# Kernel tuning notes

Measured on AMD Instinct MI355X. Metric: run time of the kernel, lower is better.

Reference implementation:

```python
import jax, jax.numpy as jnp
import numpy as np

N_EMBD = 1024
BLOCK_SIZE = 2048
ATTN_SPAN = 256
LN_EPS = 1e-5


def _band_mask(T, span, dtype):
    ones = jnp.ones((T, T), dtype=dtype)
    # tril(.,0) * (1 - tril(.,-span)) -> causal band of width `span`
    return jnp.tril(ones, 0) * (1.0 - jnp.tril(ones, -span))


def setup_inputs() -> dict:
    key = jax.random.key(0)
    k_x, k_w, k_b, k_lw = jax.random.split(key, 4)
    B, T, C = 4, BLOCK_SIZE, N_EMBD
    x = jax.random.normal(k_x, (B, T, C), dtype=jnp.float32)
    # qkv_net: Linear(C, 3C) with bias (torch default)
    lim = 1.0 / np.sqrt(C)
    W_qkv = jax.random.uniform(k_w, (C, 3 * C), minval=-lim, maxval=lim, dtype=jnp.float32)
    b_qkv = jax.random.uniform(k_b, (3 * C,), minval=-lim, maxval=lim, dtype=jnp.float32)
    ln_w = jnp.ones((C,), dtype=jnp.float32)
    ln_b = jnp.zeros((C,), dtype=jnp.float32)
    return {"x": x, "W_qkv": W_qkv, "b_qkv": b_qkv, "ln_w": ln_w, "ln_b": ln_b}


def _layer_norm(h, w, b):
    mu = jnp.mean(h, axis=-1, keepdims=True)
    var = jnp.var(h, axis=-1, keepdims=True)
    return (h - mu) * jax.lax.rsqrt(var + LN_EPS) * w + b


def reference(x, W_qkv, b_qkv, ln_w, ln_b):
    B, T, C = x.shape
    qkv = x @ W_qkv + b_qkv  # [B,T,3C]
    q, k, v = jnp.split(qkv, 3, axis=-1)
    scale = np.sqrt(C * ATTN_SPAN).astype(np.float32)
    scores = jnp.einsum('bid,bjd->bij', q, k) / scale  # [B,T,T]
    scores = scores * _band_mask(T, ATTN_SPAN, x.dtype)[None, :, :]
    out = jnp.einsum('bij,bjd->bid', scores, v)  # [B,T,C]
    return _layer_norm(out, ln_w, ln_b)
```

## Files before the change

kernel.cpp:

```cpp
#include <hip/hip_runtime.h>
#include <cstdint>
#include <cstddef>

#define N_EMBD 1024
#define T_SEQ  2048
#define NBATCH 4
#define SPAN   256
#define C3     3072

typedef float  floatx4 __attribute__((ext_vector_type(4)));
typedef __bf16 bf16x8  __attribute__((ext_vector_type(8)));

__device__ inline unsigned short f2bf(float f) {
    union { float f; unsigned u; } x; x.f = f;
    unsigned u = x.u;
    unsigned r = (u + 0x7fffu + ((u >> 16) & 1u)) >> 16;
    return (unsigned short)r;
}

typedef __attribute__((address_space(1))) const void GVOID;
typedef __attribute__((address_space(3))) void LVOID;
__device__ inline void gl2lds16(const void* g, void* l) {
    __builtin_amdgcn_global_load_lds((GVOID*)g, (LVOID*)l, 16, 0, 0);
}

__device__ inline void stage128x32(const unsigned short* g, size_t stride,
                                   unsigned short* lds, int lane, int wave) {
    const int r     = wave * 16 + (lane >> 2);
    const int chunk = (lane & 3) ^ ((r >> 1) & 3);
    const unsigned short* src = g + (size_t)r * stride + chunk * 8;
    gl2lds16(src,               &lds[(wave * 16) * 32]);
    gl2lds16(src + 64 * stride, &lds[(64 + wave * 16) * 32]);
}

__device__ inline void stage64x64(const unsigned short* g, size_t stride,
                                  unsigned short* lds, int lane, int wave) {
#pragma unroll
    for (int rnd = 0; rnd < 2; rnd++) {
        const int r = rnd * 32 + wave * 8 + (lane >> 3);
        const int chunk = (lane & 7) ^ (r & 7);
        gl2lds16(g + (size_t)r * stride + chunk * 8, &lds[(rnd * 32 + wave * 8) * 64]);
    }
}

__device__ inline void stage128x64(const unsigned short* g, size_t stride,
                                   unsigned short* lds, int lane, int wave) {
#pragma unroll
    for (int rnd = 0; rnd < 4; rnd++) {
        const int r = rnd * 32 + wave * 8 + (lane >> 3);
        const int chunk = (lane & 7) ^ (r & 7);
        gl2lds16(g + (size_t)r * stride + chunk * 8, &lds[(rnd * 32 + wave * 8) * 64]);
    }
}

__global__ __launch_bounds__(256) void k_prep(const float* __restrict__ x,
                                              unsigned short* __restrict__ Xb,
                                              const float* __restrict__ W,
                                              unsigned short* __restrict__ WbT) {
    __shared__ unsigned short t[32][33];
    if (blockIdx.x < 8192) {
        int i = (blockIdx.x * 256 + threadIdx.x) * 4;
        float4 v = *(const float4*)(x + i);
        ushort4 o;
        o.x = f2bf(v.x); o.y = f2bf(v.y); o.z = f2bf(v.z); o.w = f2bf(v.w);
        *(ushort4*)(Xb + i) = o;
    } else {
        int bid = blockIdx.x - 8192;
        int k0 = (bid & 31) * 32, n0 = (bid >> 5) * 32;
        int tx = threadIdx.x & 31, ty = threadIdx.x >> 5;
#pragma unroll
        for (int i = 0; i < 4; i++) {
            int k = k0 + ty + i * 8;
            t[ty + i * 8][tx] = f2bf(W[(size_t)k * C3 + n0 + tx]);
        }
        __syncthreads();
#pragma unroll
        for (int i = 0; i < 4; i++) {
            int n = n0 + ty + i * 8;
            WbT[(size_t)n * N_EMBD + k0 + tx] = t[tx][ty + i * 8];
        }
    }
}

__global__ __launch_bounds__(256) void k_gemm(const unsigned short* __restrict__ Xb,
                                              const unsigned short* __restrict__ WbT,
                                              const float* __restrict__ bqkv,
                                              unsigned short* __restrict__ QK,
                                              unsigned short* __restrict__ Vt) {
    __shared__ unsigned short As[4096];
    __shared__ unsigned short Bs[4096];
    const int tid = threadIdx.x, lane = tid & 63, wave = tid >> 6;
    const int bx = blockIdx.x, m0 = blockIdx.y * 128;
    const bool isV = (bx >= 16);
    const int n0 = isV ? (2048 + (bx - 16) * 128) : (bx * 128);
    const int wr = wave >> 1, wc = wave & 1;

    floatx4 acc[4][4] = {};

    const unsigned short* gA = (isV ? WbT + (size_t)n0 * N_EMBD : Xb  + (size_t)m0 * N_EMBD);
    const unsigned short* gB = (isV ? Xb  + (size_t)m0 * N_EMBD : WbT + (size_t)n0 * N_EMBD);
    const int qk = ((lane >> 4) ^ ((lane >> 1) & 3)) * 8;
    const int ra = wr * 64 + (lane & 15);
    const int rb = wc * 64 + (lane & 15);

    for (int k0 = 0; k0 < N_EMBD; k0 += 32) {
        stage128x32(gA + k0, N_EMBD, As, lane, wave);
        stage128x32(gB + k0, N_EMBD, Bs, lane, wave);
        __syncthreads();
        bf16x8 a[4], b[4];
#pragma unroll
        for (int mi = 0; mi < 4; mi++) a[mi] = *(const bf16x8*)&As[(ra + mi * 16) * 32 + qk];
#pragma unroll
        for (int ni = 0; ni < 4; ni++) b[ni] = *(const bf16x8*)&Bs[(rb + ni * 16) * 32 + qk];
#pragma unroll
        for (int mi = 0; mi < 4; mi++)
#pragma unroll
            for (int ni = 0; ni < 4; ni++)
                acc[mi][ni] = __builtin_amdgcn_mfma_f32_16x16x32_bf16(a[mi], b[ni], acc[mi][ni], 0, 0, 0);
        __syncthreads();
    }

    const int cn = lane & 15, q = lane >> 4;
    unsigned short* base = isV ? Vt : QK;
    const int rowbase = isV ? (((m0 >> 11) << 10) + (n0 - 2048)) : m0;
    const int colbase = isV ? (m0 & 2047) : n0;
#pragma unroll
    for (int mi = 0; mi < 4; mi++) {
#pragma unroll
        for (int r = 0; r < 4; r++) {
            const int arow = wr * 64 + mi * 16 + q * 4 + r;
            unsigned short* dst = base + (size_t)(rowbase + arow) * 2048 + colbase;
#pragma unroll
            for (int ni = 0; ni < 4; ni++) {
                const int acol = wc * 64 + ni * 16 + cn;
                const float bias = bqkv[n0 + (isV ? arow : acol)];
                dst[acol] = f2bf(acc[mi][ni][r] + bias);
            }
        }
    }
}

__global__ __launch_bounds__(256) void k_scores(const unsigned short* __restrict__ QK,
                                                unsigned short* __restrict__ S) {
    const int logical = (blockIdx.x & 7) * 80 + (blockIdx.x >> 3);
    const int jj = logical % 5;
    const int qb = (logical / 5) & 31;
    const int b  = logical / 160;
    const int jb = qb - 4 + jj;
    if (jb < 0) return;

    __shared__ unsigned short Qs[2][4096];
    __shared__ unsigned short Ks[2][4096];
    const int tid = threadIdx.x, lane = tid & 63, wave = tid >> 6;
    const int wr = wave >> 1, wc = wave & 1;
    const int n15 = lane & 15, q = lane >> 4;

    floatx4 acc[2][2] = {};

    const unsigned short* gQ = QK + ((size_t)(b * T_SEQ + qb * 64)) * 2048;
    const unsigned short* gK = QK + ((size_t)(b * T_SEQ + jb * 64)) * 2048 + 1024;

    for (int k0 = 0; k0 < N_EMBD; k0 += 128) {
        stage64x64(gQ + k0,      2048, Qs[0], lane, wave);
        stage64x64(gQ + k0 + 64, 2048, Qs[1], lane, wave);
        stage64x64(gK + k0,      2048, Ks[0], lane, wave);
        stage64x64(gK + k0 + 64, 2048, Ks[1], lane, wave);
        __syncthreads();
#pragma unroll
        for (int h = 0; h < 2; h++) {
#pragma unroll
            for (int s = 0; s < 2; s++) {
                bf16x8 a[2], bbf[2];
#pragma unroll
                for (int mi = 0; mi < 2; mi++) {
                    const int row = wr * 32 + mi * 16 + n15;
                    a[mi] = *(const bf16x8*)&Qs[h][row * 64 + (((s * 4 + q) ^ (row & 7)) * 8)];
                }
#pragma unroll
                for (int ni = 0; ni < 2; ni++) {
                    const int row = wc * 32 + ni * 16 + n15;
                    bbf[ni] = *(const bf16x8*)&Ks[h][row * 64 + (((s * 4 + q) ^ (row & 7)) * 8)];
                }
#pragma unroll
                for (int mi = 0; mi < 2; mi++)
#pragma unroll
                    for (int ni = 0; ni < 2; ni++)
                        acc[mi][ni] = __builtin_amdgcn_mfma_f32_16x16x32_bf16(a[mi], bbf[ni], acc[mi][ni], 0, 0, 0);
            }
        }
        __syncthreads();
    }

    unsigned short* Sb = S + (((size_t)(b * 32 + qb) * 5 + jj) << 12);
#pragma unroll
    for (int mi = 0; mi < 2; mi++)
#pragma unroll
        for (int ni = 0; ni < 2; ni++)
#pragma unroll
            for (int r = 0; r < 4; r++) {
                const int il = wr * 32 + mi * 16 + q * 4 + r;
                const int jl = wc * 32 + ni * 16 + n15;
                const int gi = qb * 64 + il, gj = jb * 64 + jl;
                const float v = ((gj <= gi) && (gj > gi - SPAN)) ? acc[mi][ni][r] * (1.0f / 512.0f) : 0.0f;
                Sb[il * 64 + jl] = f2bf(v);
            }
}

__global__ __launch_bounds__(256) void k_sv(const unsigned short* __restrict__ S,
                                            const unsigned short* __restrict__ Vt,
                                            float* __restrict__ out) {
    const int logical = (blockIdx.x & 7) * 128 + (blockIdx.x >> 3);
    const int cg = logical & 7;
    const int qb = (logical >> 3) & 31;
    const int b  = logical >> 8;
    const int c0 = cg * 128;

    __shared__ unsigned short Ss[2][4096];
    __shared__ unsigned short Vs[2][8192];
    const int tid = threadIdx.x, lane = tid & 63, wave = tid >> 6;
    const int wr = wave >> 1, wc = wave & 1;
    const int n15 = lane & 15, q = lane >> 4;

    floatx4 acc[2][4] = {};

    const size_t vbase = ((size_t)(b * 1024 + c0)) * 2048;
    const size_t sbase = ((size_t)(b * 32 + qb) * 5) << 12;

    for (int j0 = 0; j0 < 5; j0 += 2) {
        const int nv = (j0 < 4) ? 2 : 1;
        bool val[2] = {false, false};
#pragma unroll
        for (int t = 0; t < 2; t++) {
            if (t < nv && (qb - 4 + j0 + t) >= 0) {
                val[t] = true;
                stage64x64 (S + sbase + ((size_t)(j0 + t) << 12), 64, Ss[t], lane, wave);
                stage128x64(Vt + vbase + (size_t)(qb - 4 + j0 + t) * 64, 2048, Vs[t], lane, wave);
            }
        }
        __syncthreads();
#pragma unroll
        for (int t = 0; t < 2; t++) {
            if (!val[t]) continue;
#pragma unroll
            for (int s = 0; s < 2; s++) {
                bf16x8 a[2], bbf[4];
#pragma unroll
                for (int mi = 0; mi < 2; mi++) {
                    const int row = wr * 32 + mi * 16 + n15;
                    a[mi] = *(const bf16x8*)&Ss[t][row * 64 + (((s * 4 + q) ^ (row & 7)) * 8)];
                }
#pragma unroll
                for (int ni = 0; ni < 4; ni++) {
                    const int row = wc * 64 + ni * 16 + n15;
                    bbf[ni] = *(const bf16x8*)&Vs[t][row * 64 + (((s * 4 + q) ^ (row & 7)) * 8)];
                }
#pragma unroll
                for (int mi = 0; mi < 2; mi++)
#pragma unroll
                    for (int ni = 0; ni < 4; ni++)
                        acc[mi][ni] = __builtin_amdgcn_mfma_f32_16x16x32_bf16(a[mi], bbf[ni], acc[mi][ni], 0, 0, 0);
            }
        }
        __syncthreads();
    }

#pragma unroll
    for (int mi = 0; mi < 2; mi++)
#pragma unroll
        for (int ni = 0; ni < 4; ni++)
#pragma unroll
            for (int r = 0; r < 4; r++) {
                const int il = wr * 32 + mi * 16 + q * 4 + r;
                const int cl = wc * 64 + ni * 16 + n15;
                out[((size_t)(b * T_SEQ + qb * 64 + il)) * N_EMBD + c0 + cl] = acc[mi][ni][r];
            }
}

__global__ __launch_bounds__(256) void k_ln(float* __restrict__ out,
                                            const float* __restrict__ w,
                                            const float* __restrict__ bias) {
    __shared__ float red[8];
    const int t = threadIdx.x;
    float* p = out + (size_t)blockIdx.x * N_EMBD;
    float4 v = ((const float4*)p)[t];
    float s  = v.x + v.y + v.z + v.w;
    float sq = v.x * v.x + v.y * v.y + v.z * v.z + v.w * v.w;
#pragma unroll
    for (int off = 32; off; off >>= 1) {
        s  += __shfl_down(s, off, 64);
        sq += __shfl_down(sq, off, 64);
    }
    const int wave = t >> 6, lane = t & 63;
    if (lane == 0) { red[wave] = s; red[4 + wave] = sq; }
    __syncthreads();
    const float ts = red[0] + red[1] + red[2] + red[3];
    const float tq = red[4] + red[5] + red[6] + red[7];
    const float mean = ts * (1.0f / N_EMBD);
    const float var  = tq * (1.0f / N_EMBD) - mean * mean;
    const float rs = rsqrtf(var + 1e-5f);
    float4 wv = ((const float4*)w)[t];
    float4 bv = ((const float4*)bias)[t];
    float4 o;
    o.x = (v.x - mean) * rs * wv.x + bv.x;
    o.y = (v.y - mean) * rs * wv.y + bv.y;
    o.z = (v.z - mean) * rs * wv.z + bv.z;
    o.w = (v.w - mean) * rs * wv.w + bv.w;
    ((float4*)p)[t] = o;
}

extern "C" void kernel_launch(void* const* d_in, const int* in_sizes, int n_in,
                              void* d_out, int out_size, void* d_ws, size_t ws_size,
                              hipStream_t stream) {
    const float* x  = (const float*)d_in[0];
    const float* W  = (const float*)d_in[1];
    const float* bq = (const float*)d_in[2];
    const float* lw = (const float*)d_in[3];
    const float* lb = (const float*)d_in[4];
    float* out = (float*)d_out;
    char* ws = (char*)d_ws;

    unsigned short* Xb   = (unsigned short*)(ws + 0);
    unsigned short* Sbuf = (unsigned short*)(ws + 0);
    unsigned short* WbT  = (unsigned short*)(ws + 16777216);
    unsigned short* QK   = (unsigned short*)(ws + 23068672);
    unsigned short* Vt   = (unsigned short*)(ws + 56623104);

    k_prep   <<<11264,           256, 0, stream>>>(x, Xb, W, WbT);
    k_gemm   <<<dim3(24, 64),    256, 0, stream>>>(Xb, WbT, bq, QK, Vt);
    k_scores <<<640,             256, 0, stream>>>(QK, Sbuf);
    k_sv     <<<1024,            256, 0, stream>>>(Sbuf, Vt, out);
    k_ln     <<<8192,            256, 0, stream>>>(out, lw, lb);
}
```

Before: 195.8 us.

## Fuse score-times-V GEMM with LayerNorm in one full-row kernel

Replaces the separate S·V kernel and LayerNorm kernel with one kernel. Each 512-thread block computes a full 32-row by 1024-column output stripe, then does the row mean/variance reduction in registers and LDS and writes the normalized result directly. This removes the fp32 round trip of the output through global memory and one launch. V fragments are now read straight from global memory instead of being staged in LDS, and there are only 256 blocks instead of 1024, so load latency and occupancy become risks.

```diff
diff --git a/kernel.cpp b/kernel.cpp
--- a/kernel.cpp
+++ b/kernel.cpp
@@ -43,14 +43,8 @@
     }
 }
 
-__device__ inline void stage128x64(const unsigned short* g, size_t stride,
-                                   unsigned short* lds, int lane, int wave) {
-#pragma unroll
-    for (int rnd = 0; rnd < 4; rnd++) {
-        const int r = rnd * 32 + wave * 8 + (lane >> 3);
-        const int chunk = (lane & 7) ^ (r & 7);
-        gl2lds16(g + (size_t)r * stride + chunk * 8, &lds[(rnd * 32 + wave * 8) * 64]);
-    }
+__device__ inline bf16x8 frag_ld(const unsigned short* buf, int row, int ks, int q) {
+    return *(const bf16x8*)&buf[row * 64 + (((ks * 4 + q) ^ (row & 7)) * 8)];
 }
 
 __global__ __launch_bounds__(256) void k_prep(const float* __restrict__ x,
@@ -206,106 +200,95 @@
             }
 }
 
-__global__ __launch_bounds__(256) void k_sv(const unsigned short* __restrict__ S,
-                                            const unsigned short* __restrict__ Vt,
-                                            float* __restrict__ out) {
-    const int logical = (blockIdx.x & 7) * 128 + (blockIdx.x >> 3);
-    const int cg = logical & 7;
-    const int qb = (logical >> 3) & 31;
-    const int b  = logical >> 8;
-    const int c0 = cg * 128;
-
-    __shared__ unsigned short Ss[2][4096];
-    __shared__ unsigned short Vs[2][8192];
+__global__ __launch_bounds__(512) void k_svln(const unsigned short* __restrict__ S,
+                                              const unsigned short* __restrict__ Vt,
+                                              const float* __restrict__ lw,
+                                              const float* __restrict__ lb,
+                                              float* __restrict__ out) {
+    const int qh = blockIdx.x, b = blockIdx.y;
+    const int r0 = qh * 32;
+    const int qb = qh >> 1, half = qh & 1;
+    const int jt0 = qb - 4;
+
+    __shared__ unsigned short Ss[5][32 * 64];
+    __shared__ float red[2][32][8];
+
     const int tid = threadIdx.x, lane = tid & 63, wave = tid >> 6;
-    const int wr = wave >> 1, wc = wave & 1;
     const int n15 = lane & 15, q = lane >> 4;
 
-    floatx4 acc[2][4] = {};
-
-    const size_t vbase = ((size_t)(b * 1024 + c0)) * 2048;
-    const size_t sbase = ((size_t)(b * 32 + qb) * 5) << 12;
-
-    for (int j0 = 0; j0 < 5; j0 += 2) {
-        const int nv = (j0 < 4) ? 2 : 1;
-        bool val[2] = {false, false};
-#pragma unroll
-        for (int t = 0; t < 2; t++) {
-            if (t < nv && (qb - 4 + j0 + t) >= 0) {
-                val[t] = true;
-                stage64x64 (S + sbase + ((size_t)(j0 + t) << 12), 64, Ss[t], lane, wave);
-                stage128x64(Vt + vbase + (size_t)(qb - 4 + j0 + t) * 64, 2048, Vs[t], lane, wave);
-            }
-        }
-        __syncthreads();
-#pragma unroll
-        for (int t = 0; t < 2; t++) {
-            if (!val[t]) continue;
-#pragma unroll
-            for (int s = 0; s < 2; s++) {
-                bf16x8 a[2], bbf[4];
-#pragma unroll
-                for (int mi = 0; mi < 2; mi++) {
-                    const int row = wr * 32 + mi * 16 + n15;
-                    a[mi] = *(const bf16x8*)&Ss[t][row * 64 + (((s * 4 + q) ^ (row & 7)) * 8)];
-                }
-#pragma unroll
-                for (int ni = 0; ni < 4; ni++) {
-                    const int row = wc * 64 + ni * 16 + n15;
-                    bbf[ni] = *(const bf16x8*)&Vs[t][row * 64 + (((s * 4 + q) ^ (row & 7)) * 8)];
-                }
-#pragma unroll
-                for (int mi = 0; mi < 2; mi++)
-#pragma unroll
-                    for (int ni = 0; ni < 4; ni++)
-                        acc[mi][ni] = __builtin_amdgcn_mfma_f32_16x16x32_bf16(a[mi], bbf[ni], acc[mi][ni], 0, 0, 0);
-            }
-        }
-        __syncthreads();
-    }
-
-#pragma unroll
-    for (int mi = 0; mi < 2; mi++)
-#pragma unroll
-        for (int ni = 0; ni < 4; ni++)
-#pragma unroll
-            for (int r = 0; r < 4; r++) {
-                const int il = wr * 32 + mi * 16 + q * 4 + r;
-                const int cl = wc * 64 + ni * 16 + n15;
-                out[((size_t)(b * T_SEQ + qb * 64 + il)) * N_EMBD + c0 + cl] = acc[mi][ni][r];
-            }
-}
-
-__global__ __launch_bounds__(256) void k_ln(float* __restrict__ out,
-                                            const float* __restrict__ w,
-                                            const float* __restrict__ bias) {
-    __shared__ float red[8];
-    const int t = threadIdx.x;
-    float* p = out + (size_t)blockIdx.x * N_EMBD;
-    float4 v = ((const float4*)p)[t];
-    float s  = v.x + v.y + v.z + v.w;
-    float sq = v.x * v.x + v.y * v.y + v.z * v.z + v.w * v.w;
-#pragma unroll
-    for (int off = 32; off; off >>= 1) {
-        s  += __shfl_down(s, off, 64);
-        sq += __shfl_down(sq, off, 64);
-    }
-    const int wave = t >> 6, lane = t & 63;
-    if (lane == 0) { red[wave] = s; red[4 + wave] = sq; }
+    const unsigned short* Sg = S + (((size_t)(b * 32 + qb) * 5) << 12) + half * 2048;
+#pragma unroll
+    for (int rnd = 0; rnd < 3; ++rnd) {
+        const int tl = rnd * 2 + (wave >> 2);
+        if (tl < 5 && (jt0 + tl) >= 0) {
+            const int r = (wave & 3) * 8 + (lane >> 3);
+            const int chunk = (lane & 7) ^ (r & 7);
+            gl2lds16(Sg + ((size_t)tl << 12) + (size_t)r * 64 + chunk * 8,
+                     &Ss[tl][((wave & 3) * 8) * 64]);
+        }
+    }
     __syncthreads();
-    const float ts = red[0] + red[1] + red[2] + red[3];
-    const float tq = red[4] + red[5] + red[6] + red[7];
-    const float mean = ts * (1.0f / N_EMBD);
-    const float var  = tq * (1.0f / N_EMBD) - mean * mean;
-    const float rs = rsqrtf(var + 1e-5f);
-    float4 wv = ((const float4*)w)[t];
-    float4 bv = ((const float4*)bias)[t];
-    float4 o;
-    o.x = (v.x - mean) * rs * wv.x + bv.x;
-    o.y = (v.y - mean) * rs * wv.y + bv.y;
-    o.z = (v.z - mean) * rs * wv.z + bv.z;
-    o.w = (v.w - mean) * rs * wv.w + bv.w;
-    ((float4*)p)[t] = o;
+
+    floatx4 acc[2][8] = {};
+    const unsigned short* gV = Vt + (size_t)(b * 1024 + wave * 128) * 2048;
+#pragma unroll
+    for (int jtl = 0; jtl < 5; ++jtl) {
+        const int jt = jt0 + jtl;
+        if (jt < 0) continue;
+#pragma unroll
+        for (int ks = 0; ks < 2; ++ks) {
+            bf16x8 a0 = frag_ld(Ss[jtl], n15, ks, q);
+            bf16x8 a1 = frag_ld(Ss[jtl], 16 + n15, ks, q);
+            const size_t tb = (size_t)jt * 64 + ks * 32 + q * 8;
+#pragma unroll
+            for (int nt = 0; nt < 8; ++nt) {
+                const bf16x8 bv = *(const bf16x8*)(gV + (size_t)(nt * 16 + n15) * 2048 + tb);
+                acc[0][nt] = __builtin_amdgcn_mfma_f32_16x16x32_bf16(a0, bv, acc[0][nt], 0, 0, 0);
+                acc[1][nt] = __builtin_amdgcn_mfma_f32_16x16x32_bf16(a1, bv, acc[1][nt], 0, 0, 0);
+            }
+        }
+    }
+
+#pragma unroll
+    for (int mi = 0; mi < 2; ++mi)
+#pragma unroll
+        for (int r = 0; r < 4; ++r) {
+            float s = 0.0f, sq = 0.0f;
+#pragma unroll
+            for (int nt = 0; nt < 8; ++nt) {
+                const float v = acc[mi][nt][r];
+                s += v; sq += v * v;
+            }
+#pragma unroll
+            for (int off = 1; off < 16; off <<= 1) {
+                s  += __shfl_xor(s, off, 64);
+                sq += __shfl_xor(sq, off, 64);
+            }
+            if (n15 == 0) {
+                red[0][mi * 16 + q * 4 + r][wave] = s;
+                red[1][mi * 16 + q * 4 + r][wave] = sq;
+            }
+        }
+    __syncthreads();
+
+    float* po = out + (size_t)(b * T_SEQ + r0) * N_EMBD;
+#pragma unroll
+    for (int mi = 0; mi < 2; ++mi)
+#pragma unroll
+        for (int r = 0; r < 4; ++r) {
+            const int row = mi * 16 + q * 4 + r;
+            float ts = 0.0f, tq = 0.0f;
+#pragma unroll
+            for (int w = 0; w < 8; ++w) { ts += red[0][row][w]; tq += red[1][row][w]; }
+            const float mean = ts * (1.0f / N_EMBD);
+            const float var  = tq * (1.0f / N_EMBD) - mean * mean;
+            const float rs = rsqrtf(var + 1e-5f);
+#pragma unroll
+            for (int nt = 0; nt < 8; ++nt) {
+                const int c = wave * 128 + nt * 16 + n15;
+                po[(size_t)row * N_EMBD + c] = (acc[mi][nt][r] - mean) * rs * lw[c] + lb[c];
+            }
+        }
 }
 
 extern "C" void kernel_launch(void* const* d_in, const int* in_sizes, int n_in,
@@ -325,9 +308,8 @@
     unsigned short* QK   = (unsigned short*)(ws + 23068672);
     unsigned short* Vt   = (unsigned short*)(ws + 56623104);
 
-    k_prep   <<<11264,           256, 0, stream>>>(x, Xb, W, WbT);
-    k_gemm   <<<dim3(24, 64),    256, 0, stream>>>(Xb, WbT, bq, QK, Vt);
-    k_scores <<<640,             256, 0, stream>>>(QK, Sbuf);
-    k_sv     <<<1024,            256, 0, stream>>>(Sbuf, Vt, out);
-    k_ln     <<<8192,            256, 0, stream>>>(out, lw, lb);
-}
+    k_prep   <<<11264,        256, 0, stream>>>(x, Xb, W, WbT);
+    k_gemm   <<<dim3(24, 64), 256, 0, stream>>>(Xb, WbT, bq, QK, Vt);
+    k_scores <<<640,          256, 0, stream>>>(QK, Sbuf);
+    k_svln   <<<dim3(64, 4),  512, 0, stream>>>(Sbuf, Vt, lw, lb, out);
+}
```

After: 210.4 us. +7.4%, slower.

## Pair key blocks per scores workgroup and remap GEMM grid for XCD locality

Applied to the files above, without the earlier changes.

The scores kernel now handles two adjacent 64-wide key blocks per workgroup, so one staged Q tile is shared by both. Each wave column owns one key block with a 2x4 MFMA tile, and the grid shrinks from 640 to 384 blocks. The QKV GEMM moves to a 1D grid with an XCD-aware block index remap, so neighbouring tiles that share operands land on the same die. Costs: larger LDS use per scores block, and idle waves when one of the paired key blocks is invalid or missing (the fifth band block).

```diff
diff --git a/kernel.cpp b/kernel.cpp
--- a/kernel.cpp
+++ b/kernel.cpp
@@ -51,6 +51,10 @@
         const int chunk = (lane & 7) ^ (r & 7);
         gl2lds16(g + (size_t)r * stride + chunk * 8, &lds[(rnd * 32 + wave * 8) * 64]);
     }
+}
+
+__device__ inline bf16x8 frag_ld(const unsigned short* buf, int row, int ks, int q) {
+    return *(const bf16x8*)&buf[row * 64 + (((ks * 4 + q) ^ (row & 7)) * 8)];
 }
 
 __global__ __launch_bounds__(256) void k_prep(const float* __restrict__ x,
@@ -90,7 +94,9 @@
     __shared__ unsigned short As[4096];
     __shared__ unsigned short Bs[4096];
     const int tid = threadIdx.x, lane = tid & 63, wave = tid >> 6;
-    const int bx = blockIdx.x, m0 = blockIdx.y * 128;
+    const int logical = (blockIdx.x & 7) * 192 + (blockIdx.x >> 3);
+    const int bx = logical % 24;
+    const int m0 = (logical / 24) * 128;
     const bool isV = (bx >= 16);
     const int n0 = isV ? (2048 + (bx - 16) * 128) : (bx * 128);
     const int wr = wave >> 1, wc = wave & 1;
@@ -142,64 +148,75 @@
 
 __global__ __launch_bounds__(256) void k_scores(const unsigned short* __restrict__ QK,
                                                 unsigned short* __restrict__ S) {
-    const int logical = (blockIdx.x & 7) * 80 + (blockIdx.x >> 3);
-    const int jj = logical % 5;
-    const int qb = (logical / 5) & 31;
-    const int b  = logical / 160;
-    const int jb = qb - 4 + jj;
-    if (jb < 0) return;
+    const int logical = (blockIdx.x & 7) * 48 + (blockIdx.x >> 3);
+    const int p  = logical % 3;
+    const int qb = (logical / 3) & 31;
+    const int b  = logical / 96;
+    const int jj0 = 2 * p;
+    const int jb0 = qb - 4 + jj0;
+    const bool v0 = (jb0 >= 0);
+    const bool v1 = (p < 2) && (jb0 + 1 >= 0);
+    if (!v0 && !v1) return;
 
     __shared__ unsigned short Qs[2][4096];
-    __shared__ unsigned short Ks[2][4096];
+    __shared__ unsigned short Ks[2][2][4096];
     const int tid = threadIdx.x, lane = tid & 63, wave = tid >> 6;
     const int wr = wave >> 1, wc = wave & 1;
     const int n15 = lane & 15, q = lane >> 4;
-
-    floatx4 acc[2][2] = {};
-
-    const unsigned short* gQ = QK + ((size_t)(b * T_SEQ + qb * 64)) * 2048;
-    const unsigned short* gK = QK + ((size_t)(b * T_SEQ + jb * 64)) * 2048 + 1024;
+    const bool myv = wc ? v1 : v0;
+
+    floatx4 acc[2][4] = {};
+
+    const unsigned short* gQ  = QK + ((size_t)(b * T_SEQ + qb * 64)) * 2048;
+    const unsigned short* gK0 = QK + ((size_t)(b * T_SEQ + jb0 * 64)) * 2048 + 1024;
+    const unsigned short* gK1 = gK0 + (size_t)64 * 2048;
 
     for (int k0 = 0; k0 < N_EMBD; k0 += 128) {
         stage64x64(gQ + k0,      2048, Qs[0], lane, wave);
         stage64x64(gQ + k0 + 64, 2048, Qs[1], lane, wave);
-        stage64x64(gK + k0,      2048, Ks[0], lane, wave);
-        stage64x64(gK + k0 + 64, 2048, Ks[1], lane, wave);
-        __syncthreads();
-#pragma unroll
-        for (int h = 0; h < 2; h++) {
-#pragma unroll
-            for (int s = 0; s < 2; s++) {
-                bf16x8 a[2], bbf[2];
-#pragma unroll
-                for (int mi = 0; mi < 2; mi++) {
-                    const int row = wr * 32 + mi * 16 + n15;
-                    a[mi] = *(const bf16x8*)&Qs[h][row * 64 + (((s * 4 + q) ^ (row & 7)) * 8)];
+        if (v0) {
+            stage64x64(gK0 + k0,      2048, Ks[0][0], lane, wave);
+            stage64x64(gK0 + k0 + 64, 2048, Ks[1][0], lane, wave);
+        }
+        if (v1) {
+            stage64x64(gK1 + k0,      2048, Ks[0][1], lane, wave);
+            stage64x64(gK1 + k0 + 64, 2048, Ks[1][1], lane, wave);
+        }
+        __syncthreads();
+        if (myv) {
+#pragma unroll
+            for (int h = 0; h < 2; h++) {
+#pragma unroll
+                for (int s = 0; s < 2; s++) {
+                    bf16x8 a[2], bbf[4];
+#pragma unroll
+                    for (int mi = 0; mi < 2; mi++)
+                        a[mi] = frag_ld(Qs[h], wr * 32 + mi * 16 + n15, s, q);
+#pragma unroll
+                    for (int ni = 0; ni < 4; ni++)
+                        bbf[ni] = frag_ld(Ks[h][wc], ni * 16 + n15, s, q);
+#pragma unroll
+                    for (int mi = 0; mi < 2; mi++)
+#pragma unroll
+                        for (int ni = 0; ni < 4; ni++)
+                            acc[mi][ni] = __builtin_amdgcn_mfma_f32_16x16x32_bf16(a[mi], bbf[ni], acc[mi][ni], 0, 0, 0);
                 }
-#pragma unroll
-                for (int ni = 0; ni < 2; ni++) {
-                    const int row = wc * 32 + ni * 16 + n15;
-                    bbf[ni] = *(const bf16x8*)&Ks[h][row * 64 + (((s * 4 + q) ^ (row & 7)) * 8)];
-                }
-#pragma unroll
-                for (int mi = 0; mi < 2; mi++)
-#pragma unroll
-                    for (int ni = 0; ni < 2; ni++)
-                        acc[mi][ni] = __builtin_amdgcn_mfma_f32_16x16x32_bf16(a[mi], bbf[ni], acc[mi][ni], 0, 0, 0);
-            }
-        }
-        __syncthreads();
-    }
-
+            }
+        }
+        __syncthreads();
+    }
+
+    if (!myv) return;
+    const int jb = jb0 + wc, jj = jj0 + wc;
     unsigned short* Sb = S + (((size_t)(b * 32 + qb) * 5 + jj) << 12);
 #pragma unroll
     for (int mi = 0; mi < 2; mi++)
 #pragma unroll
-        for (int ni = 0; ni < 2; ni++)
+        for (int ni = 0; ni < 4; ni++)
 #pragma unroll
             for (int r = 0; r < 4; r++) {
                 const int il = wr * 32 + mi * 16 + q * 4 + r;
-                const int jl = wc * 32 + ni * 16 + n15;
+                const int jl = ni * 16 + n15;
                 const int gi = qb * 64 + il, gj = jb * 64 + jl;
                 const float v = ((gj <= gi) && (gj > gi - SPAN)) ? acc[mi][ni][r] * (1.0f / 512.0f) : 0.0f;
                 Sb[il * 64 + jl] = f2bf(v);
@@ -325,9 +342,9 @@
     unsigned short* QK   = (unsigned short*)(ws + 23068672);
     unsigned short* Vt   = (unsigned short*)(ws + 56623104);
 
-    k_prep   <<<11264,           256, 0, stream>>>(x, Xb, W, WbT);
-    k_gemm   <<<dim3(24, 64),    256, 0, stream>>>(Xb, WbT, bq, QK, Vt);
-    k_scores <<<640,             256, 0, stream>>>(QK, Sbuf);
-    k_sv     <<<1024,            256, 0, stream>>>(Sbuf, Vt, out);
-    k_ln     <<<8192,            256, 0, stream>>>(out, lw, lb);
-}
+    k_prep   <<<11264, 256, 0, stream>>>(x, Xb, W, WbT);
+    k_gemm   <<<1536,  256, 0, stream>>>(Xb, WbT, bq, QK, Vt);
+    k_scores <<<384,   256, 0, stream>>>(QK, Sbuf);
+    k_sv     <<<1024,  256, 0, stream>>>(Sbuf, Vt, out);
+    k_ln     <<<8192,  256, 0, stream>>>(out, lw, lb);
+}
```

New measurement: 203.2 us. 3.8% more time.
